# Optimization experiments

Hardware: AMD Instinct MI355X
Metric: run time of the kernel (lower is better)

## Reference

```python
import jax, jax.numpy as jnp
import numpy as np

B, T, C, HEADS = 4, 2305, 384, 6
BN_EPS = 1e-5


def setup_inputs() -> dict:
    key = jax.random.key(0)
    ks = jax.random.split(key, 24)
    d = {
        'x': jax.random.normal(ks[0], (B, T, C), dtype=jnp.float32),
        'h': 48,
        'w': 48,
        # depthwise conv kernels (groups=C, no bias): OIHW with I=1
        'kq': jax.random.normal(ks[1], (C, 1, 3, 3), dtype=jnp.float32) * 0.1,
        'kk': jax.random.normal(ks[2], (C, 1, 3, 3), dtype=jnp.float32) * 0.1,
        'kv': jax.random.normal(ks[3], (C, 1, 3, 3), dtype=jnp.float32) * 0.1,
        # BatchNorm (eval mode) params per projection: gamma, beta, running_mean, running_var
        'gq': jax.random.normal(ks[4], (C,), dtype=jnp.float32) * 0.1 + 1.0,
        'bq': jax.random.normal(ks[5], (C,), dtype=jnp.float32) * 0.1,
        'mq': jax.random.normal(ks[6], (C,), dtype=jnp.float32) * 0.1,
        'vq': jax.random.uniform(ks[7], (C,), dtype=jnp.float32) + 0.5,
        'gk': jax.random.normal(ks[8], (C,), dtype=jnp.float32) * 0.1 + 1.0,
        'bk': jax.random.normal(ks[9], (C,), dtype=jnp.float32) * 0.1,
        'mk': jax.random.normal(ks[10], (C,), dtype=jnp.float32) * 0.1,
        'vk': jax.random.uniform(ks[11], (C,), dtype=jnp.float32) + 0.5,
        'gv': jax.random.normal(ks[12], (C,), dtype=jnp.float32) * 0.1 + 1.0,
        'bv': jax.random.normal(ks[13], (C,), dtype=jnp.float32) * 0.1,
        'mv': jax.random.normal(ks[14], (C,), dtype=jnp.float32) * 0.1,
        'vv': jax.random.uniform(ks[15], (C,), dtype=jnp.float32) + 0.5,
        # Linear weights, torch convention [out, in]; qkv_bias=False
        'Wq': jax.random.normal(ks[16], (C, C), dtype=jnp.float32) / np.sqrt(C),
        'Wk': jax.random.normal(ks[17], (C, C), dtype=jnp.float32) / np.sqrt(C),
        'Wv': jax.random.normal(ks[18], (C, C), dtype=jnp.float32) / np.sqrt(C),
        'Wo': jax.random.normal(ks[19], (C, C), dtype=jnp.float32) / np.sqrt(C),
        'bo': jax.random.normal(ks[20], (C,), dtype=jnp.float32) * 0.01,
    }
    return d


def _dw_bn(xi, kern, gamma, beta, mean, var, h, w):
    # xi: [B, C, h, w]; depthwise 3x3 conv, stride 1, pad 1, then eval-mode BN
    y = jax.lax.conv_general_dilated(
        xi, kern, window_strides=(1, 1), padding=((1, 1), (1, 1)),
        feature_group_count=C, dimension_numbers=('NCHW', 'OIHW', 'NCHW'))
    scale = (gamma / jnp.sqrt(var + BN_EPS))[None, :, None, None]
    y = (y - mean[None, :, None, None]) * scale + beta[None, :, None, None]
    # b c h w -> b (h w) c
    return y.transpose(0, 2, 3, 1).reshape(y.shape[0], h * w, C)


def _forward(x, kq, kk, kv, gq, bq, mq, vq, gk, bk, mk, vk, gv, bv, mv, vv,
             Wq, Wk, Wv, Wo, bo, h, w):
    b, t, c = x.shape
    scale = c ** (-0.5)  # note: dim**-0.5, NOT head_dim**-0.5 (as in source)
    cls_tok, xs = x[:, :1], x[:, 1:]
    xi = xs.reshape(b, h, w, c).transpose(0, 3, 1, 2)  # b (h w) c -> b c h w
    q = jnp.concatenate([cls_tok, _dw_bn(xi, kq, gq, bq, mq, vq, h, w)], axis=1)
    k = jnp.concatenate([cls_tok, _dw_bn(xi, kk, gk, bk, mk, vk, h, w)], axis=1)
    v = jnp.concatenate([cls_tok, _dw_bn(xi, kv, gv, bv, mv, vv, h, w)], axis=1)
    dh = c // HEADS
    q = (q @ Wq.T).reshape(b, t, HEADS, dh).transpose(0, 2, 1, 3)  # bhtd
    k = (k @ Wk.T).reshape(b, t, HEADS, dh).transpose(0, 2, 1, 3)
    v = (v @ Wv.T).reshape(b, t, HEADS, dh).transpose(0, 2, 1, 3)
    attn = jax.nn.softmax(jnp.einsum('bhld,bhtd->bhlt', q, k) * scale, axis=-1)
    out = jnp.einsum('bhlt,bhtd->bhld', attn, v)
    out = out.transpose(0, 2, 1, 3).reshape(b, t, c)
    return out @ Wo.T + bo


def reference(x, kq, kk, kv, gq, bq, mq, vq, gk, bk, mk, vk, gv, bv, mv, vv,
              Wq, Wk, Wv, Wo, bo, h, w):
    return _forward(x, kq, kk, kv, gq, bq, mq, vq, gk, bk, mk, vk, gv, bv,
                    mv, vv, Wq, Wk, Wv, Wo, bo, h, w)
```

## Files before the change

### kernel.cpp

```cpp
#include <hip/hip_runtime.h>
#include <hip/hip_bf16.h>

#define BN 4
#define TT 2305
#define CC 384
#define HH 6
#define DH 64
#define GW 48
#define BH (BN*HH)
#define TP 2368
#define TQP 2560
#define MF 9220
#define MP 9344
#define MB2 73
#define C2 0.07362223f

typedef __hip_bfloat16 bf16;
typedef __attribute__((ext_vector_type(8))) short short8;
typedef __attribute__((ext_vector_type(4))) float floatx4;
typedef __attribute__((ext_vector_type(16))) float floatx16;

#define MFMA16(a,b,c) __builtin_amdgcn_mfma_f32_16x16x32_bf16((a),(b),(c),0,0,0)
#define MFMA32(a,b,c) __builtin_amdgcn_mfma_f32_32x32x16_bf16((a),(b),(c),0,0,0)

__device__ __forceinline__ unsigned pack2(float a, float b) {
    bf16 lo = __float2bfloat16(a);
    bf16 hi = __float2bfloat16(b);
    unsigned short ul = *reinterpret_cast<unsigned short*>(&lo);
    unsigned short uh = *reinterpret_cast<unsigned short*>(&hi);
    return (unsigned)ul | ((unsigned)uh << 16);
}
__device__ __forceinline__ float bu2f(unsigned u16) {
    unsigned v = u16 << 16;
    return *reinterpret_cast<float*>(&v);
}

__global__ __launch_bounds__(384)
void conv_bn(const float* __restrict__ x,
             const float* __restrict__ kq, const float* __restrict__ kk, const float* __restrict__ kv,
             const float* __restrict__ gq, const float* __restrict__ bq, const float* __restrict__ mq, const float* __restrict__ vq,
             const float* __restrict__ gk, const float* __restrict__ bk, const float* __restrict__ mk, const float* __restrict__ vk,
             const float* __restrict__ gv, const float* __restrict__ bv, const float* __restrict__ mv, const float* __restrict__ vv,
             bf16* __restrict__ cq, bf16* __restrict__ ck, bf16* __restrict__ cv)
{
    const int n = blockIdx.x;
    const int b = n / 289;
    const int t0 = (n % 289) * 8;
    const int c = threadIdx.x;
    const size_t xbase = (size_t)b * TT * CC;

    const float sq = gq[c] * rsqrtf(vq[c] + 1e-5f), oq = bq[c] - mq[c] * sq;
    const float sk = gk[c] * rsqrtf(vk[c] + 1e-5f), ok = bk[c] - mk[c] * sk;
    const float sv = gv[c] * rsqrtf(vv[c] + 1e-5f), ov = bv[c] - mv[c] * sv;
    float wq9[9], wk9[9], wv9[9];
    #pragma unroll
    for (int u = 0; u < 9; u++) {
        wq9[u] = kq[c * 9 + u]; wk9[u] = kk[c * 9 + u]; wv9[u] = kv[c * 9 + u];
    }

    for (int g = 0; g < 8; g++) {
        const int t = t0 + g;
        if (t >= TT) break;
        const size_t mrow = (size_t)(b * TT + t) * CC + c;
        if (t == 0) {
            bf16 xv = __float2bfloat16(x[xbase + c]);
            cq[mrow] = xv; ck[mrow] = xv; cv[mrow] = xv;
        } else {
            const int s = t - 1, i = s / GW, j = s % GW;
            float aq = 0.f, ak = 0.f, av = 0.f;
            #pragma unroll
            for (int di = 0; di < 3; di++) {
                int ii = i + di - 1;
                if (ii < 0 || ii >= GW) continue;
                #pragma unroll
                for (int dj = 0; dj < 3; dj++) {
                    int jj = j + dj - 1;
                    if (jj < 0 || jj >= GW) continue;
                    float xv = x[xbase + (size_t)(1 + ii * GW + jj) * CC + c];
                    int u = di * 3 + dj;
                    aq += xv * wq9[u]; ak += xv * wk9[u]; av += xv * wv9[u];
                }
            }
            cq[mrow] = __float2bfloat16(aq * sq + oq);
            ck[mrow] = __float2bfloat16(ak * sk + ok);
            cv[mrow] = __float2bfloat16(av * sv + ov);
        }
    }
}

__global__ __launch_bounds__(256)
void qkv_gemm(const bf16* __restrict__ cq, const bf16* __restrict__ ck, const bf16* __restrict__ cv,
              const bf16* __restrict__ Wq, const bf16* __restrict__ Wk, const bf16* __restrict__ Wv,
              bf16* __restrict__ q, bf16* __restrict__ k, bf16* __restrict__ vT)
{
    const int m0 = blockIdx.x * 128;
    const int n0 = blockIdx.y * 64;
    const int w = threadIdx.x >> 6, lane = threadIdx.x & 63;
    const int lm = lane & 15, q4 = lane >> 4;
    const int which = n0 / CC;
    const int obase = n0 % CC;
    const bf16* A = (which == 0) ? cq : (which == 1) ? ck : cv;
    const bf16* W = (which == 0) ? Wq : (which == 1) ? Wk : Wv;

    const size_t ar0 = (size_t)(m0 + w * 16 + lm) * CC;
    floatx4 acc[2][4];
    #pragma unroll
    for (int st = 0; st < 2; st++)
        #pragma unroll
        for (int n = 0; n < 4; n++) acc[st][n] = (floatx4){0.f, 0.f, 0.f, 0.f};

    #pragma unroll 4
    for (int kc = 0; kc < CC / 32; kc++) {
        short8 a0 = *(const short8*)(A + ar0 + kc * 32 + q4 * 8);
        short8 a1 = *(const short8*)(A + ar0 + (size_t)64 * CC + kc * 32 + q4 * 8);
        #pragma unroll
        for (int n = 0; n < 4; n++) {
            short8 bfr = *(const short8*)(W + (size_t)(obase + n * 16 + lm) * CC + kc * 32 + q4 * 8);
            acc[0][n] = MFMA16(a0, bfr, acc[0][n]);
            acc[1][n] = MFMA16(a1, bfr, acc[1][n]);
        }
    }

    #pragma unroll
    for (int st = 0; st < 2; st++)
        #pragma unroll
        for (int n = 0; n < 4; n++) {
            const int o = obase + n * 16 + lm;
            const int h = o >> 6, d = o & 63;
            #pragma unroll
            for (int r = 0; r < 4; r++) {
                const int m = m0 + st * 64 + w * 16 + q4 * 4 + r;
                if (m >= MF) continue;
                const int b = m / TT, t = m % TT;
                bf16 val = __float2bfloat16(acc[st][n][r]);
                if (which == 0)
                    q[((size_t)(b * HH + h) * TQP + t) * DH + d] = val;
                else if (which == 1)
                    k[((size_t)(b * HH + h) * TP + t) * DH + d] = val;
                else
                    vT[((size_t)(b * HH + h) * DH + d) * TP + t] = val;
            }
        }
}

__global__ __launch_bounds__(256, 2)
void flash(const bf16* __restrict__ q, const bf16* __restrict__ k,
           const bf16* __restrict__ vT, bf16* __restrict__ OP, float* __restrict__ ML)
{
    const int bh = blockIdx.y;
    const int z = blockIdx.z;
    const int tid = threadIdx.x;
    const int w = tid >> 6, lane = tid & 63;
    const int q31 = lane & 31, hh = lane >> 5;
    const int q0 = blockIdx.x * 256 + w * 64;
    const size_t kbase = (size_t)bh * TP * DH;
    const size_t qbase = (size_t)bh * TQP * DH;

    __shared__ __align__(16) bf16 Ks[2][64 * 64];
    __shared__ __align__(16) bf16 Vs[2][64 * 64];

    short8 qf[2][4];
    #pragma unroll
    for (int s = 0; s < 2; s++) {
        const bf16* qrow = q + qbase + (size_t)(q0 + s * 32 + q31) * DH;
        #pragma unroll
        for (int kc = 0; kc < 4; kc++)
            qf[s][kc] = *(const short8*)(qrow + kc * 16 + hh * 8);
    }

    floatx16 of[2][2];
    #pragma unroll
    for (int s = 0; s < 2; s++)
        #pragma unroll
        for (int dt = 0; dt < 2; dt++)
            #pragma unroll
            for (int r = 0; r < 16; r++) of[s][dt][r] = 0.f;
    float m2[2] = {-1e30f, -1e30f}, lsum[2] = {0.f, 0.f};

    const int tstart = z ? 19 : 0;
    const int tend   = z ? 37 : 19;

    const int sidx = tid, sidx2 = tid + 256;
    const int tr0 = sidx >> 3,  c80 = sidx & 7;
    const int tr1 = sidx2 >> 3, c81 = sidx2 & 7;
    const int so0 = tr0 * 64 + ((c80 ^ (tr0 & 7)) * 8);
    const int so1 = tr1 * 64 + ((c81 ^ (tr1 & 7)) * 8);

    uint4 kreg[2], vreg[2];
    {
        const int t0 = tstart * 64;
        kreg[0] = *(const uint4*)(k + kbase + (size_t)(t0 + tr0) * DH + c80 * 8);
        vreg[0] = *(const uint4*)(vT + kbase + (size_t)tr0 * TP + t0 + c80 * 8);
        kreg[1] = *(const uint4*)(k + kbase + (size_t)(t0 + tr1) * DH + c81 * 8);
        vreg[1] = *(const uint4*)(vT + kbase + (size_t)tr1 * TP + t0 + c81 * 8);
    }
    *(uint4*)&Ks[0][so0] = kreg[0];
    *(uint4*)&Vs[0][so0] = vreg[0];
    *(uint4*)&Ks[0][so1] = kreg[1];
    *(uint4*)&Vs[0][so1] = vreg[1];

    for (int tc = tstart; tc < tend; tc++) {
        const int cur = (tc - tstart) & 1;
        const int t0 = tc * 64;
        __syncthreads();
        const bool more = (tc + 1 < tend);
        if (more) {
            const int t1 = t0 + 64;
            kreg[0] = *(const uint4*)(k + kbase + (size_t)(t1 + tr0) * DH + c80 * 8);
            vreg[0] = *(const uint4*)(vT + kbase + (size_t)tr0 * TP + t1 + c80 * 8);
            kreg[1] = *(const uint4*)(k + kbase + (size_t)(t1 + tr1) * DH + c81 * 8);
            vreg[1] = *(const uint4*)(vT + kbase + (size_t)tr1 * TP + t1 + c81 * 8);
        }
        const bf16* Kc = Ks[cur];
        const bf16* Vc = Vs[cur];

        short8 ka[2][4], va[2][4];
        #pragma unroll
        for (int mt = 0; mt < 2; mt++)
            #pragma unroll
            for (int kc = 0; kc < 4; kc++) {
                const int row = mt * 32 + q31, c = 2 * kc + hh;
                ka[mt][kc] = *(const short8*)&Kc[row * 64 + ((c ^ (row & 7)) * 8)];
                va[mt][kc] = *(const short8*)&Vc[row * 64 + ((c ^ (row & 7)) * 8)];
            }
        const bool tail = (t0 + 64 > TT);

        #pragma unroll
        for (int s = 0; s < 2; s++) {
            floatx16 sv[2];
            #pragma unroll
            for (int mt = 0; mt < 2; mt++)
                #pragma unroll
                for (int r = 0; r < 16; r++) sv[mt][r] = 0.f;
            #pragma unroll
            for (int kc = 0; kc < 4; kc++) {
                sv[0] = MFMA32(ka[0][kc], qf[s][kc], sv[0]);
                sv[1] = MFMA32(ka[1][kc], qf[s][kc], sv[1]);
            }
            if (tail) {
                #pragma unroll
                for (int mt = 0; mt < 2; mt++)
                    #pragma unroll
                    for (int r = 0; r < 16; r++) {
                        const int tl = t0 + mt * 32 + (r & 3) + 8 * (r >> 2) + 4 * hh;
                        if (tl >= TT) sv[mt][r] = -1e30f;
                    }
            }
            float rm = sv[0][0];
            #pragma unroll
            for (int r = 1; r < 16; r++) rm = fmaxf(rm, sv[0][r]);
            #pragma unroll
            for (int r = 0; r < 16; r++) rm = fmaxf(rm, sv[1][r]);
            rm = fmaxf(rm, __shfl_xor(rm, 32));
            const float mn = fmaxf(m2[s], rm * C2);
            const float alpha = __builtin_amdgcn_exp2f(m2[s] - mn);
            m2[s] = mn;
            const float negm = -mn;
            float rs = 0.f;
            unsigned pk[2][8];
            #pragma unroll
            for (int mt = 0; mt < 2; mt++)
                #pragma unroll
                for (int p = 0; p < 8; p++) {
                    const float p0 = __builtin_amdgcn_exp2f(fmaf(sv[mt][2 * p], C2, negm));
                    const float p1 = __builtin_amdgcn_exp2f(fmaf(sv[mt][2 * p + 1], C2, negm));
                    rs += p0 + p1;
                    pk[mt][p] = pack2(p0, p1);
                }
            rs += __shfl_xor(rs, 32);
            lsum[s] = lsum[s] * alpha + rs;
            #pragma unroll
            for (int dt = 0; dt < 2; dt++)
                #pragma unroll
                for (int r = 0; r < 16; r++) of[s][dt][r] *= alpha;

            #pragma unroll
            for (int kc = 0; kc < 4; kc++) {
                const int u0 = 2 * kc, u1 = 2 * kc + 1;
                const unsigned P0a = pk[u0 >> 2][2 * (u0 & 3)];
                const unsigned P0b = pk[u0 >> 2][2 * (u0 & 3) + 1];
                const unsigned P1a = pk[u1 >> 2][2 * (u1 & 3)];
                const unsigned P1b = pk[u1 >> 2][2 * (u1 & 3) + 1];
                const unsigned X1 = hh ? P0a : P1a;
                const unsigned X2 = hh ? P0b : P1b;
                const unsigned Y1 = __shfl_xor(X1, 32);
                const unsigned Y2 = __shfl_xor(X2, 32);
                unsigned dw[4];
                dw[0] = hh ? Y1 : P0a;
                dw[1] = hh ? Y2 : P0b;
                dw[2] = hh ? P1a : Y1;
                dw[3] = hh ? P1b : Y2;
                short8 pb = *reinterpret_cast<short8*>(dw);
                of[s][0] = MFMA32(va[0][kc], pb, of[s][0]);
                of[s][1] = MFMA32(va[1][kc], pb, of[s][1]);
            }
        }

        if (more) {
            bf16* Kn = Ks[1 - cur];
            bf16* Vn = Vs[1 - cur];
            *(uint4*)&Kn[so0] = kreg[0];
            *(uint4*)&Vn[so0] = vreg[0];
            *(uint4*)&Kn[so1] = kreg[1];
            *(uint4*)&Vn[so1] = vreg[1];
        }
    }

    #pragma unroll
    for (int s = 0; s < 2; s++) {
        const int qrow = q0 + s * 32 + q31;
        if (qrow >= TT) continue;
        bf16* orow = OP + ((size_t)(z * BH + bh) * 2560 + qrow) * DH;
        #pragma unroll
        for (int dt = 0; dt < 2; dt++)
            #pragma unroll
            for (int p = 0; p < 4; p++) {
                const int d = dt * 32 + 8 * p + 4 * hh;
                unsigned lo = pack2(of[s][dt][4 * p], of[s][dt][4 * p + 1]);
                unsigned hi = pack2(of[s][dt][4 * p + 2], of[s][dt][4 * p + 3]);
                uint2 st = {lo, hi};
                *(uint2*)(orow + d) = st;
            }
        if (hh == 0) {
            float2 ml = {m2[s], lsum[s]};
            *(float2*)&ML[((size_t)(z * BH + bh) * 2560 + qrow) * 2] = ml;
        }
    }
}

__global__ __launch_bounds__(256)
void merge(const bf16* __restrict__ OP, const float* __restrict__ ML,
           bf16* __restrict__ att)
{
    const int idx = blockIdx.x * 256 + threadIdx.x;
    if (idx >= BH * TT * 16) return;
    const int quad = idx & 15;
    const int pair = idx >> 4;
    const int bh = pair / TT, row = pair % TT;
    const int b = bh / HH, h = bh % HH;
    const int d0 = quad * 4;

    const float2 ml0 = *(const float2*)&ML[((size_t)bh * 2560 + row) * 2];
    const float2 ml1 = *(const float2*)&ML[((size_t)(BH + bh) * 2560 + row) * 2];
    const float M = fmaxf(ml0.x, ml1.x);
    const float w0 = __builtin_amdgcn_exp2f(ml0.x - M);
    const float w1 = __builtin_amdgcn_exp2f(ml1.x - M);
    const float inv = 1.f / (ml0.y * w0 + ml1.y * w1);
    const float s0 = w0 * inv, s1 = w1 * inv;

    const uint2 a = *(const uint2*)&OP[((size_t)bh * 2560 + row) * DH + d0];
    const uint2 c = *(const uint2*)&OP[((size_t)(BH + bh) * 2560 + row) * DH + d0];
    float o0 = bu2f(a.x & 0xffffu) * s0 + bu2f(c.x & 0xffffu) * s1;
    float o1 = bu2f(a.x >> 16)     * s0 + bu2f(c.x >> 16)     * s1;
    float o2 = bu2f(a.y & 0xffffu) * s0 + bu2f(c.y & 0xffffu) * s1;
    float o3 = bu2f(a.y >> 16)     * s0 + bu2f(c.y >> 16)     * s1;

    uint2 st = {pack2(o0, o1), pack2(o2, o3)};
    *(uint2*)&att[((size_t)(b * TT + row) * CC) + h * DH + d0] = st;
}

__global__ __launch_bounds__(256)
void out_gemm(const bf16* __restrict__ att, const bf16* __restrict__ Wo_bf,
              const float* __restrict__ bo, float* __restrict__ out)
{
    const int m0 = blockIdx.x * 128;
    const int n0 = blockIdx.y * 64;
    const int w = threadIdx.x >> 6, lane = threadIdx.x & 63;
    const int lm = lane & 15, q4 = lane >> 4;

    const size_t ar0 = (size_t)(m0 + w * 16 + lm) * CC;
    floatx4 acc[2][4];
    #pragma unroll
    for (int st = 0; st < 2; st++)
        #pragma unroll
        for (int n = 0; n < 4; n++) acc[st][n] = (floatx4){0.f, 0.f, 0.f, 0.f};

    #pragma unroll 4
    for (int kc = 0; kc < CC / 32; kc++) {
        short8 a0 = *(const short8*)(att + ar0 + kc * 32 + q4 * 8);
        short8 a1 = *(const short8*)(att + ar0 + (size_t)64 * CC + kc * 32 + q4 * 8);
        #pragma unroll
        for (int n = 0; n < 4; n++) {
            short8 bfr = *(const short8*)(Wo_bf + (size_t)(n0 + n * 16 + lm) * CC + kc * 32 + q4 * 8);
            acc[0][n] = MFMA16(a0, bfr, acc[0][n]);
            acc[1][n] = MFMA16(a1, bfr, acc[1][n]);
        }
    }

    #pragma unroll
    for (int st = 0; st < 2; st++)
        #pragma unroll
        for (int n = 0; n < 4; n++) {
            const int o = n0 + n * 16 + lm;
            const float bias = bo[o];
            #pragma unroll
            for (int r = 0; r < 4; r++) {
                const int m = m0 + st * 64 + w * 16 + q4 * 4 + r;
                if (m < MF) out[(size_t)m * CC + o] = acc[st][n][r] + bias;
            }
        }
}

__global__ __launch_bounds__(256)
void cvt_w(const float* __restrict__ Wq, const float* __restrict__ Wk,
           const float* __restrict__ Wv, const float* __restrict__ Wo,
           bf16* __restrict__ q, bf16* __restrict__ k,
           bf16* __restrict__ v, bf16* __restrict__ o)
{
    const int i = blockIdx.x * 256 + threadIdx.x;
    if (i < CC * CC) {
        q[i] = __float2bfloat16(Wq[i]);
        k[i] = __float2bfloat16(Wk[i]);
        v[i] = __float2bfloat16(Wv[i]);
        o[i] = __float2bfloat16(Wo[i]);
    }
}

extern "C" void kernel_launch(void* const* d_in, const int* in_sizes, int n_in,
                              void* d_out, int out_size, void* d_ws, size_t ws_size,
                              hipStream_t stream)
{
    const float* x  = (const float*)d_in[0];
    const float* kq = (const float*)d_in[3];
    const float* kk = (const float*)d_in[4];
    const float* kv = (const float*)d_in[5];
    const float* gq = (const float*)d_in[6];
    const float* bq = (const float*)d_in[7];
    const float* mq = (const float*)d_in[8];
    const float* vq = (const float*)d_in[9];
    const float* gk = (const float*)d_in[10];
    const float* bk = (const float*)d_in[11];
    const float* mk = (const float*)d_in[12];
    const float* vk = (const float*)d_in[13];
    const float* gv = (const float*)d_in[14];
    const float* bv = (const float*)d_in[15];
    const float* mv = (const float*)d_in[16];
    const float* vv = (const float*)d_in[17];
    const float* Wq = (const float*)d_in[18];
    const float* Wk = (const float*)d_in[19];
    const float* Wv = (const float*)d_in[20];
    const float* Wo = (const float*)d_in[21];
    const float* bo = (const float*)d_in[22];

    char* ws = (char*)d_ws;
    const size_t SZ_CONV = (size_t)MP * CC * 2;
    const size_t SZ_Q    = (size_t)BH * TQP * DH * 2;
    const size_t SZ_K    = (size_t)BH * TP * DH * 2;
    const size_t SZ_W    = (size_t)CC * CC * 2;
    size_t off = 0;
    bf16* cq   = (bf16*)(ws + off); off += SZ_CONV;
    bf16* ck   = (bf16*)(ws + off); off += SZ_CONV;
    bf16* cv   = (bf16*)(ws + off); off += SZ_CONV;
    bf16* qb   = (bf16*)(ws + off); off += SZ_Q;
    bf16* kb   = (bf16*)(ws + off); off += SZ_K;
    bf16* vTb  = (bf16*)(ws + off); off += SZ_K;
    bf16* attb = (bf16*)(ws + off); off += SZ_CONV;
    bf16* wqb  = (bf16*)(ws + off); off += SZ_W;
    bf16* wkb  = (bf16*)(ws + off); off += SZ_W;
    bf16* wvb  = (bf16*)(ws + off); off += SZ_W;
    bf16* wob  = (bf16*)(ws + off); off += SZ_W;

    bf16*  OP = (bf16*)ws;
    float* ML = (float*)(ws + 2 * (size_t)BH * 2560 * DH * 2);

    cvt_w<<<(CC * CC + 255) / 256, 256, 0, stream>>>(Wq, Wk, Wv, Wo, wqb, wkb, wvb, wob);
    conv_bn<<<BN * 289, 384, 0, stream>>>(x, kq, kk, kv,
                                          gq, bq, mq, vq,
                                          gk, bk, mk, vk,
                                          gv, bv, mv, vv, cq, ck, cv);
    qkv_gemm<<<dim3(MB2, 18), 256, 0, stream>>>(cq, ck, cv, wqb, wkb, wvb, qb, kb, vTb);
    flash<<<dim3(10, BH, 2), 256, 0, stream>>>(qb, kb, vTb, OP, ML);
    merge<<<(BH * TT * 16 + 255) / 256, 256, 0, stream>>>(OP, ML, attb);
    out_gemm<<<dim3(MB2, 6), 256, 0, stream>>>(attb, wob, bo, (float*)d_out);
}
```

Baseline: 299.4 us.

## Split flash attention three ways, retile QKV GEMM, fuse weight cast into conv

The weight fp32-to-bf16 conversion is folded into the conv_bn kernel, which removes one launch. The QKV GEMM now tiles 256 rows per batch and transposes V through shared memory so vT is written with coalesced 16-byte stores. Flash attention splits the key range three ways instead of two to fill more compute units, and it skips the output rescale when no row in the wave gets a new max. The merge kernel is generalized to NSPL partials. In exchange there is more partial-output traffic and merge work, and the larger GEMM tile raises register use.

New measurement: 309.1 us. +3.2%, slower.

```diff
diff --git a/kernel.cpp b/kernel.cpp
--- a/kernel.cpp
+++ b/kernel.cpp
@@ -13,6 +13,7 @@
 #define MF 9220
 #define MP 9344
 #define MB2 73
+#define NSPL 3
 #define C2 0.07362223f
 
 typedef __hip_bfloat16 bf16;
@@ -41,8 +42,22 @@
              const float* __restrict__ gq, const float* __restrict__ bq, const float* __restrict__ mq, const float* __restrict__ vq,
              const float* __restrict__ gk, const float* __restrict__ bk, const float* __restrict__ mk, const float* __restrict__ vk,
              const float* __restrict__ gv, const float* __restrict__ bv, const float* __restrict__ mv, const float* __restrict__ vv,
+             const float* __restrict__ Wq, const float* __restrict__ Wk,
+             const float* __restrict__ Wv, const float* __restrict__ Wo,
+             bf16* __restrict__ wqb, bf16* __restrict__ wkb,
+             bf16* __restrict__ wvb, bf16* __restrict__ wob,
              bf16* __restrict__ cq, bf16* __restrict__ ck, bf16* __restrict__ cv)
 {
+    {
+        const int i = blockIdx.x * 384 + threadIdx.x;
+        if (i < CC * CC) {
+            wqb[i] = __float2bfloat16(Wq[i]);
+            wkb[i] = __float2bfloat16(Wk[i]);
+            wvb[i] = __float2bfloat16(Wv[i]);
+            wob[i] = __float2bfloat16(Wo[i]);
+        }
+    }
+
     const int n = blockIdx.x;
     const int b = n / 289;
     const int t0 = (n % 289) * 8;
@@ -93,7 +108,9 @@
               const bf16* __restrict__ Wq, const bf16* __restrict__ Wk, const bf16* __restrict__ Wv,
               bf16* __restrict__ q, bf16* __restrict__ k, bf16* __restrict__ vT)
 {
-    const int m0 = blockIdx.x * 128;
+    const int bt = blockIdx.x;
+    const int b = bt / 10;
+    const int m0 = (bt % 10) * 256;
     const int n0 = blockIdx.y * 64;
     const int w = threadIdx.x >> 6, lane = threadIdx.x & 63;
     const int lm = lane & 15, q4 = lane >> 4;
@@ -102,45 +119,84 @@
     const bf16* A = (which == 0) ? cq : (which == 1) ? ck : cv;
     const bf16* W = (which == 0) ? Wq : (which == 1) ? Wk : Wv;
 
-    const size_t ar0 = (size_t)(m0 + w * 16 + lm) * CC;
-    floatx4 acc[2][4];
-    #pragma unroll
-    for (int st = 0; st < 2; st++)
+    __shared__ __align__(16) bf16 TR[64 * 264];
+
+    size_t arow[4];
+    #pragma unroll
+    for (int st = 0; st < 4; st++) {
+        int t = m0 + st * 64 + w * 16 + lm;
+        if (t >= TT) t = TT - 1;
+        arow[st] = (size_t)(b * TT + t) * CC;
+    }
+
+    floatx4 acc[4][4];
+    #pragma unroll
+    for (int st = 0; st < 4; st++)
         #pragma unroll
         for (int n = 0; n < 4; n++) acc[st][n] = (floatx4){0.f, 0.f, 0.f, 0.f};
 
-    #pragma unroll 4
+    #pragma unroll 2
     for (int kc = 0; kc < CC / 32; kc++) {
-        short8 a0 = *(const short8*)(A + ar0 + kc * 32 + q4 * 8);
-        short8 a1 = *(const short8*)(A + ar0 + (size_t)64 * CC + kc * 32 + q4 * 8);
+        short8 a[4];
+        #pragma unroll
+        for (int st = 0; st < 4; st++)
+            a[st] = *(const short8*)(A + arow[st] + kc * 32 + q4 * 8);
         #pragma unroll
         for (int n = 0; n < 4; n++) {
             short8 bfr = *(const short8*)(W + (size_t)(obase + n * 16 + lm) * CC + kc * 32 + q4 * 8);
-            acc[0][n] = MFMA16(a0, bfr, acc[0][n]);
-            acc[1][n] = MFMA16(a1, bfr, acc[1][n]);
-        }
-    }
-
-    #pragma unroll
-    for (int st = 0; st < 2; st++)
-        #pragma unroll
-        for (int n = 0; n < 4; n++) {
-            const int o = obase + n * 16 + lm;
-            const int h = o >> 6, d = o & 63;
-            #pragma unroll
-            for (int r = 0; r < 4; r++) {
-                const int m = m0 + st * 64 + w * 16 + q4 * 4 + r;
-                if (m >= MF) continue;
-                const int b = m / TT, t = m % TT;
-                bf16 val = __float2bfloat16(acc[st][n][r]);
-                if (which == 0)
-                    q[((size_t)(b * HH + h) * TQP + t) * DH + d] = val;
-                else if (which == 1)
-                    k[((size_t)(b * HH + h) * TP + t) * DH + d] = val;
-                else
-                    vT[((size_t)(b * HH + h) * DH + d) * TP + t] = val;
-            }
-        }
+            #pragma unroll
+            for (int st = 0; st < 4; st++)
+                acc[st][n] = MFMA16(a[st], bfr, acc[st][n]);
+        }
+    }
+
+    if (which == 2) {
+        #pragma unroll
+        for (int st = 0; st < 4; st++)
+            #pragma unroll
+            for (int n = 0; n < 4; n++) {
+                const int ol = n * 16 + lm;
+                const int ml = st * 64 + w * 16 + q4 * 4;
+                uint2 pkd = { pack2(acc[st][n][0], acc[st][n][1]),
+                              pack2(acc[st][n][2], acc[st][n][3]) };
+                *(uint2*)&TR[ol * 264 + ml] = pkd;
+            }
+        __syncthreads();
+        const int h = obase >> 6;
+        const int o = threadIdx.x >> 2;
+        const int seg = threadIdx.x & 3;
+        const size_t vrow = ((size_t)(b * HH + h) * DH + o) * TP;
+        #pragma unroll
+        for (int j = 0; j < 8; j++) {
+            const int ml = seg * 64 + j * 8;
+            const int t = m0 + ml;
+            uint4 val = *(const uint4*)&TR[o * 264 + ml];
+            if (t + 8 <= TT) {
+                *(uint4*)(vT + vrow + t) = val;
+            } else if (t < TT) {
+                const bf16* pv = (const bf16*)&val;
+                for (int e = 0; e < 8 && t + e < TT; e++) vT[vrow + t + e] = pv[e];
+            }
+        }
+    } else {
+        #pragma unroll
+        for (int st = 0; st < 4; st++)
+            #pragma unroll
+            for (int n = 0; n < 4; n++) {
+                const int o = obase + n * 16 + lm;
+                const int h = o >> 6, d = o & 63;
+                #pragma unroll
+                for (int r = 0; r < 4; r++) {
+                    const int t = m0 + st * 64 + w * 16 + q4 * 4 + r;
+                    if (t >= TT) continue;
+                    bf16 val = __float2bfloat16(acc[st][n][r]);
+                    if (which == 0)
+                        q[((size_t)(b * HH + h) * TQP + t) * DH + d] = val;
+                    else
+                        k[((size_t)(b * HH + h) * TP + t) * DH + d] = val;
+                }
+            }
+    }
 }
 
 __global__ __launch_bounds__(256, 2)
@@ -177,12 +233,11 @@
             for (int r = 0; r < 16; r++) of[s][dt][r] = 0.f;
     float m2[2] = {-1e30f, -1e30f}, lsum[2] = {0.f, 0.f};
 
-    const int tstart = z ? 19 : 0;
-    const int tend   = z ? 37 : 19;
-
-    const int sidx = tid, sidx2 = tid + 256;
-    const int tr0 = sidx >> 3,  c80 = sidx & 7;
-    const int tr1 = sidx2 >> 3, c81 = sidx2 & 7;
+    const int tstart = (z == 0) ? 0 : (z == 1) ? 13 : 25;
+    const int tend   = (z == 0) ? 13 : (z == 1) ? 25 : 37;
+
+    const int tr0 = tid >> 3,          c80 = tid & 7;
+    const int tr1 = (tid + 256) >> 3,  c81 = tid & 7;
     const int so0 = tr0 * 64 + ((c80 ^ (tr0 & 7)) * 8);
     const int so1 = tr1 * 64 + ((c81 ^ (tr1 & 7)) * 8);
 
@@ -253,8 +308,7 @@
             for (int r = 0; r < 16; r++) rm = fmaxf(rm, sv[1][r]);
             rm = fmaxf(rm, __shfl_xor(rm, 32));
             const float mn = fmaxf(m2[s], rm * C2);
-            const float alpha = __builtin_amdgcn_exp2f(m2[s] - mn);
-            m2[s] = mn;
+            const bool newmax = mn > m2[s];
             const float negm = -mn;
             float rs = 0.f;
             unsigned pk[2][8];
@@ -268,11 +322,17 @@
                     pk[mt][p] = pack2(p0, p1);
                 }
             rs += __shfl_xor(rs, 32);
-            lsum[s] = lsum[s] * alpha + rs;
-            #pragma unroll
-            for (int dt = 0; dt < 2; dt++)
+            if (__any(newmax)) {
+                const float alpha = __builtin_amdgcn_exp2f(m2[s] - mn);
+                lsum[s] = lsum[s] * alpha + rs;
                 #pragma unroll
-                for (int r = 0; r < 16; r++) of[s][dt][r] *= alpha;
+                for (int dt = 0; dt < 2; dt++)
+                    #pragma unroll
+                    for (int r = 0; r < 16; r++) of[s][dt][r] *= alpha;
+            } else {
+                lsum[s] += rs;
+            }
+            m2[s] = mn;
 
             #pragma unroll
             for (int kc = 0; kc < 4; kc++) {
@@ -310,7 +370,7 @@
     for (int s = 0; s < 2; s++) {
         const int qrow = q0 + s * 32 + q31;
         if (qrow >= TT) continue;
-        bf16* orow = OP + ((size_t)(z * BH + bh) * 2560 + qrow) * DH;
+        bf16* orow = OP + ((size_t)(z * BH + bh) * TT + qrow) * DH;
         #pragma unroll
         for (int dt = 0; dt < 2; dt++)
             #pragma unroll
@@ -323,7 +383,7 @@
             }
         if (hh == 0) {
             float2 ml = {m2[s], lsum[s]};
-            *(float2*)&ML[((size_t)(z * BH + bh) * 2560 + qrow) * 2] = ml;
+            *(float2*)&ML[((size_t)(z * BH + bh) * TT + qrow) * 2] = ml;
         }
     }
 }
@@ -340,21 +400,31 @@
     const int b = bh / HH, h = bh % HH;
     const int d0 = quad * 4;
 
-    const float2 ml0 = *(const float2*)&ML[((size_t)bh * 2560 + row) * 2];
-    const float2 ml1 = *(const float2*)&ML[((size_t)(BH + bh) * 2560 + row) * 2];
-    const float M = fmaxf(ml0.x, ml1.x);
-    const float w0 = __builtin_amdgcn_exp2f(ml0.x - M);
-    const float w1 = __builtin_amdgcn_exp2f(ml1.x - M);
-    const float inv = 1.f / (ml0.y * w0 + ml1.y * w1);
-    const float s0 = w0 * inv, s1 = w1 * inv;
-
-    const uint2 a = *(const uint2*)&OP[((size_t)bh * 2560 + row) * DH + d0];
-    const uint2 c = *(const uint2*)&OP[((size_t)(BH + bh) * 2560 + row) * DH + d0];
-    float o0 = bu2f(a.x & 0xffffu) * s0 + bu2f(c.x & 0xffffu) * s1;
-    float o1 = bu2f(a.x >> 16)     * s0 + bu2f(c.x >> 16)     * s1;
-    float o2 = bu2f(a.y & 0xffffu) * s0 + bu2f(c.y & 0xffffu) * s1;
-    float o3 = bu2f(a.y >> 16)     * s0 + bu2f(c.y >> 16)     * s1;
-
+    float2 ml[NSPL];
+    #pragma unroll
+    for (int z = 0; z < NSPL; z++)
+        ml[z] = *(const float2*)&ML[((size_t)(z * BH + bh) * TT + row) * 2];
+    float M = ml[0].x;
+    #pragma unroll
+    for (int z = 1; z < NSPL; z++) M = fmaxf(M, ml[z].x);
+    float wz[NSPL], den = 0.f;
+    #pragma unroll
+    for (int z = 0; z < NSPL; z++) {
+        wz[z] = __builtin_amdgcn_exp2f(ml[z].x - M);
+        den += ml[z].y * wz[z];
+    }
+    const float inv = 1.f / den;
+
+    float o0 = 0.f, o1 = 0.f, o2 = 0.f, o3 = 0.f;
+    #pragma unroll
+    for (int z = 0; z < NSPL; z++) {
+        const float s = wz[z] * inv;
+        const uint2 a = *(const uint2*)&OP[((size_t)(z * BH + bh) * TT + row) * DH + d0];
+        o0 += bu2f(a.x & 0xffffu) * s;
+        o1 += bu2f(a.x >> 16)     * s;
+        o2 += bu2f(a.y & 0xffffu) * s;
+        o3 += bu2f(a.y >> 16)     * s;
+    }
     uint2 st = {pack2(o0, o1), pack2(o2, o3)};
     *(uint2*)&att[((size_t)(b * TT + row) * CC) + h * DH + d0] = st;
 }
@@ -399,21 +469,6 @@
                 if (m < MF) out[(size_t)m * CC + o] = acc[st][n][r] + bias;
             }
         }
-}
-
-__global__ __launch_bounds__(256)
-void cvt_w(const float* __restrict__ Wq, const float* __restrict__ Wk,
-           const float* __restrict__ Wv, const float* __restrict__ Wo,
-           bf16* __restrict__ q, bf16* __restrict__ k,
-           bf16* __restrict__ v, bf16* __restrict__ o)
-{
-    const int i = blockIdx.x * 256 + threadIdx.x;
-    if (i < CC * CC) {
-        q[i] = __float2bfloat16(Wq[i]);
-        k[i] = __float2bfloat16(Wk[i]);
-        v[i] = __float2bfloat16(Wv[i]);
-        o[i] = __float2bfloat16(Wo[i]);
-    }
 }
 
 extern "C" void kernel_launch(void* const* d_in, const int* in_sizes, int n_in,
@@ -459,17 +514,18 @@
     bf16* wkb  = (bf16*)(ws + off); off += SZ_W;
     bf16* wvb  = (bf16*)(ws + off); off += SZ_W;
     bf16* wob  = (bf16*)(ws + off); off += SZ_W;
-
     bf16*  OP = (bf16*)ws;
-    float* ML = (float*)(ws + 2 * (size_t)BH * 2560 * DH * 2);
-
-    cvt_w<<<(CC * CC + 255) / 256, 256, 0, stream>>>(Wq, Wk, Wv, Wo, wqb, wkb, wvb, wob);
+    float* ML = (float*)(ws + off); off += (size_t)NSPL * BH * TT * 2 * 4;
+
     conv_bn<<<BN * 289, 384, 0, stream>>>(x, kq, kk, kv,
                                           gq, bq, mq, vq,
                                           gk, bk, mk, vk,
-                                          gv, bv, mv, vv, cq, ck, cv);
-    qkv_gemm<<<dim3(MB2, 18), 256, 0, stream>>>(cq, ck, cv, wqb, wkb, wvb, qb, kb, vTb);
-    flash<<<dim3(10, BH, 2), 256, 0, stream>>>(qb, kb, vTb, OP, ML);
+                                          gv, bv, mv, vv,
+                                          Wq, Wk, Wv, Wo,
+                                          wqb, wkb, wvb, wob,
+                                          cq, ck, cv);
+    qkv_gemm<<<dim3(40, 18), 256, 0, stream>>>(cq, ck, cv, wqb, wkb, wvb, qb, kb, vTb);
+    flash<<<dim3(10, BH, NSPL), 256, 0, stream>>>(qb, kb, vTb, OP, ML);
     merge<<<(BH * TT * 16 + 255) / 256, 256, 0, stream>>>(OP, ML, attb);
     out_gemm<<<dim3(MB2, 6), 256, 0, stream>>>(attb, wob, bo, (float*)d_out);
 }
```
